# Performance work log

Measured on AMD Instinct MI355X. Metric: run time of the kernel, lower is better.

## Reference

```python
import jax, jax.numpy as jnp
import numpy as np

B, S, P, I = 32, 64, 32, 256
NF, H, L = 4, 512, 2
OUT = 2
INITRANGE = 0.1
assert NF * I == 2 * H  # layer-2 GRU input dim equals layer-1 input dim


def setup_inputs() -> dict:
    key = jax.random.key(0)
    ks = jax.random.split(key, 12)
    u = lambda k, shape: jax.random.uniform(k, shape, jnp.float32, -INITRANGE, INITRANGE)
    return {
        "inputs": jax.random.normal(ks[0], (B, S, P, I), jnp.float32),
        "inputs_demoip": jax.random.normal(ks[1], (B, 3), jnp.float32),
        "conv_w": u(ks[2], (NF, I)),            # Conv1d(1, NF, kernel=I) == dot product
        "conv_b": u(ks[3], (NF,)),
        "conv2_w": u(ks[4], (2 * H,)),          # Conv1d(1, 1, kernel=2H) == dot product
        "conv2_b": u(ks[5], (1,)),
        "wih": u(ks[6], (L, 2, 3 * H, NF * I)),  # [layer, dir, 3H, in]
        "whh": u(ks[7], (L, 2, 3 * H, H)),
        "bih": u(ks[8], (L, 2, 3 * H)),
        "bhh": u(ks[9], (L, 2, 3 * H)),
        "lin_w": u(ks[10], (OUT, 2 * H + 3)),
        "lin_b": u(ks[11], (OUT,)),
        "batch_size": B,
    }


def _gru_dir(x, wih, whh, bih, bhh, reverse):
    """One direction of a torch-style GRU. x: [B,S,in] -> [B,S,H]."""
    gx = jnp.einsum('bsi,gi->bsg', x, wih) + bih  # precompute input gates [B,S,3H]
    if reverse:
        gx = gx[:, ::-1]
    h0 = jnp.zeros((x.shape[0], H), x.dtype)

    def step(h, gxt):
        gh = h @ whh.T + bhh
        xr, xz, xn = jnp.split(gxt, 3, axis=-1)
        hr, hz, hn = jnp.split(gh, 3, axis=-1)
        r = jax.nn.sigmoid(xr + hr)
        z = jax.nn.sigmoid(xz + hz)
        n = jnp.tanh(xn + r * hn)
        h_new = (1.0 - z) * n + z * h
        return h_new, h_new

    _, ys = jax.lax.scan(step, h0, gx.transpose(1, 0, 2))
    ys = ys.transpose(1, 0, 2)  # [B,S,H]
    if reverse:
        ys = ys[:, ::-1]
    return ys


def reference(inputs, inputs_demoip, conv_w, conv_b, conv2_w, conv2_b,
              wih, whh, bih, bhh, lin_w, lin_b, batch_size):
    # --- convolutional attention embedding (kernel spans full input -> dot product) ---
    scores = jnp.einsum('bspi,fi->bsfp', inputs, conv_w) + conv_b[None, None, :, None]
    conv_wts = jax.nn.softmax(scores, axis=-1)                    # softmax over pad dim
    vec = jnp.einsum('bsfp,bspi->bsfi', conv_wts, inputs)         # [B,S,NF,I]
    embedding = vec.reshape(batch_size, S, NF * I)                # [B,S,NF*I]

    # --- stacked bidirectional GRU (eval mode: dropout omitted) ---
    x = embedding
    for l in range(L):
        f = _gru_dir(x, wih[l, 0], whh[l, 0], bih[l, 0], bhh[l, 0], False)
        b = _gru_dir(x, wih[l, 1], whh[l, 1], bih[l, 1], bhh[l, 1], True)
        x = jnp.concatenate([f, b], axis=-1)
    states = x                                                    # [B,S,2H]

    # --- second attention (conv2 kernel spans 2H -> dot product per step) ---
    alpha = jax.nn.softmax(states @ conv2_w + conv2_b[0], axis=1)  # [B,S]
    context = jnp.einsum('bs,bsh->bh', alpha, states)              # [B,2H]

    context_v2 = jnp.concatenate([context, inputs_demoip], axis=1)  # [B,2H+3]
    out = jax.nn.softmax(context_v2 @ lin_w.T + lin_b, axis=1)      # [B,OUT]
    return out, conv_wts, states, context, alpha
```

## Files before the change

kernel.cpp:

```cpp
#include <hip/hip_runtime.h>

typedef __attribute__((ext_vector_type(8))) short s8v;
typedef __attribute__((ext_vector_type(8))) __bf16 bf8v;
typedef __attribute__((ext_vector_type(4))) float f32x4;

#define DEVINL __device__ __forceinline__

DEVINL unsigned short f2bf(float f) {
    unsigned int x = __float_as_uint(f);
    unsigned int r = (x + 0x7FFFu + ((x >> 16) & 1u)) >> 16;
    return (unsigned short)r;
}

DEVINL f32x4 mfma16(s8v a, s8v b, f32x4 c) {
    return __builtin_amdgcn_mfma_f32_16x16x32_bf16(
        __builtin_bit_cast(bf8v, a), __builtin_bit_cast(bf8v, b), c, 0, 0, 0);
}

#define WS_CTR   0
#define WS_HBUF  4096
#define WS_ZERO_BYTES 266240
#define WS_WIH   266240
#define WS_WHH   (WS_WIH + 12582912)
#define WS_EMB   (WS_WHH + 6291456)
#define WS_ST1   (WS_EMB + 4194304)
#define WS_GX    (WS_ST1 + 4194304)

__global__ __launch_bounds__(256) void k_cvt(const float* __restrict__ in,
                                             unsigned short* __restrict__ out, int n) {
    int i0 = (blockIdx.x * 256 + threadIdx.x) * 8;
    if (i0 + 8 > n) return;
    f32x4 a = *(const f32x4*)(in + i0);
    f32x4 b = *(const f32x4*)(in + i0 + 4);
    s8v o;
    o[0] = (short)f2bf(a[0]); o[1] = (short)f2bf(a[1]);
    o[2] = (short)f2bf(a[2]); o[3] = (short)f2bf(a[3]);
    o[4] = (short)f2bf(b[0]); o[5] = (short)f2bf(b[1]);
    o[6] = (short)f2bf(b[2]); o[7] = (short)f2bf(b[3]);
    *(s8v*)(out + i0) = o;
}

__global__ __launch_bounds__(256) void k_conv(const float* __restrict__ inp,
                                              const float* __restrict__ conv_w,
                                              const float* __restrict__ conv_b,
                                              float* __restrict__ wts_out,
                                              unsigned short* __restrict__ emb) {
    const int bs = blockIdx.x, tid = threadIdx.x;
    __shared__ float xs[32][260];
    __shared__ float sc[4][32];
    __shared__ float wts[4][32];
    const float* x = inp + (size_t)bs * 8192;
    {
        int p = tid >> 3, i0 = (tid & 7) * 32;
        const float* src = x + p * 256 + i0;
        float* dst = &xs[p][i0];
#pragma unroll
        for (int j = 0; j < 32; j += 4) *(f32x4*)(dst + j) = *(const f32x4*)(src + j);
    }
    __syncthreads();
    {
        int p = tid >> 3, o = tid & 7;
        float s0 = 0, s1 = 0, s2 = 0, s3 = 0;
        const float* xp = &xs[p][o * 32];
#pragma unroll
        for (int j = 0; j < 32; j += 4) {
            f32x4 v  = *(const f32x4*)(xp + j);
            f32x4 w0 = *(const f32x4*)(conv_w + o * 32 + j);
            f32x4 w1 = *(const f32x4*)(conv_w + 256 + o * 32 + j);
            f32x4 w2 = *(const f32x4*)(conv_w + 512 + o * 32 + j);
            f32x4 w3 = *(const f32x4*)(conv_w + 768 + o * 32 + j);
#pragma unroll
            for (int q = 0; q < 4; ++q) {
                s0 += v[q] * w0[q]; s1 += v[q] * w1[q];
                s2 += v[q] * w2[q]; s3 += v[q] * w3[q];
            }
        }
#pragma unroll
        for (int d = 4; d; d >>= 1) {
            s0 += __shfl_down(s0, d, 8); s1 += __shfl_down(s1, d, 8);
            s2 += __shfl_down(s2, d, 8); s3 += __shfl_down(s3, d, 8);
        }
        if (o == 0) {
            sc[0][p] = s0 + conv_b[0]; sc[1][p] = s1 + conv_b[1];
            sc[2][p] = s2 + conv_b[2]; sc[3][p] = s3 + conv_b[3];
        }
    }
    __syncthreads();
    if (tid < 4) {
        float mx = -1e30f;
        for (int p = 0; p < 32; ++p) mx = fmaxf(mx, sc[tid][p]);
        float sm = 0.f;
        for (int p = 0; p < 32; ++p) { float e = __expf(sc[tid][p] - mx); wts[tid][p] = e; sm += e; }
        float inv = 1.f / sm;
        for (int p = 0; p < 32; ++p) wts[tid][p] *= inv;
    }
    __syncthreads();
    if (tid < 128) wts_out[(size_t)bs * 128 + tid] = wts[tid >> 5][tid & 31];
    {
        float a0 = 0, a1 = 0, a2 = 0, a3 = 0;
#pragma unroll 8
        for (int p = 0; p < 32; ++p) {
            float v = xs[p][tid];
            a0 += wts[0][p] * v; a1 += wts[1][p] * v;
            a2 += wts[2][p] * v; a3 += wts[3][p] * v;
        }
        unsigned short* e = emb + (size_t)bs * 1024;
        e[tid] = f2bf(a0); e[256 + tid] = f2bf(a1);
        e[512 + tid] = f2bf(a2); e[768 + tid] = f2bf(a3);
    }
}

__global__ __launch_bounds__(256, 2) void k_gemm(const unsigned short* __restrict__ A,
                                                 const unsigned short* __restrict__ B,
                                                 const float* __restrict__ bias,
                                                 const float* __restrict__ bias2,
                                                 float* __restrict__ C,
                                                 int M, int N, int K) {
    const int bm = blockIdx.y * 64, bn = blockIdx.x * 64;
    const int tid = threadIdx.x, w = tid >> 6, l = tid & 63;
    const int wm = (w >> 1) * 32, wn = (w & 1) * 32;
    __shared__ unsigned short As[64][72];
    __shared__ unsigned short Bs[64][72];
    f32x4 acc[2][2] = {};
    const int sr = tid >> 2;
    const int sk = (tid & 3) * 8;
    const int am = (l & 15), ak = (l >> 4) * 8;
    for (int k0 = 0; k0 < K; k0 += 64) {
        s8v a0 = *(const s8v*)(A + (size_t)(bm + sr) * K + k0 + sk);
        s8v a1 = *(const s8v*)(A + (size_t)(bm + sr) * K + k0 + sk + 32);
        s8v b0 = *(const s8v*)(B + (size_t)(bn + sr) * K + k0 + sk);
        s8v b1 = *(const s8v*)(B + (size_t)(bn + sr) * K + k0 + sk + 32);
        __syncthreads();
        *(s8v*)&As[sr][sk] = a0; *(s8v*)&As[sr][sk + 32] = a1;
        *(s8v*)&Bs[sr][sk] = b0; *(s8v*)&Bs[sr][sk + 32] = b1;
        __syncthreads();
#pragma unroll
        for (int kk = 0; kk < 64; kk += 32) {
            s8v fa0 = *(const s8v*)&As[wm + am][kk + ak];
            s8v fa1 = *(const s8v*)&As[wm + 16 + am][kk + ak];
            s8v fb0 = *(const s8v*)&Bs[wn + am][kk + ak];
            s8v fb1 = *(const s8v*)&Bs[wn + 16 + am][kk + ak];
            acc[0][0] = mfma16(fa0, fb0, acc[0][0]);
            acc[0][1] = mfma16(fa0, fb1, acc[0][1]);
            acc[1][0] = mfma16(fa1, fb0, acc[1][0]);
            acc[1][1] = mfma16(fa1, fb1, acc[1][1]);
        }
    }
#pragma unroll
    for (int mt = 0; mt < 2; ++mt)
#pragma unroll
        for (int nt = 0; nt < 2; ++nt)
#pragma unroll
            for (int r = 0; r < 4; ++r) {
                int row = bm + wm + mt * 16 + (l >> 4) * 4 + r;
                int col = bn + wn + nt * 16 + (l & 15);
                int gg = col >> 9;
                float b2 = (gg != 2 && gg != 5 && bias2) ? bias2[col] : 0.f;
                C[(size_t)row * N + col] = acc[mt][nt][r] + bias[col] + b2;
            }
}

__global__ __launch_bounds__(256, 1) void k_scan(const float* __restrict__ gx,
                                                 const unsigned short* __restrict__ whh,
                                                 const float* __restrict__ bhh,
                                                 unsigned short* __restrict__ hbuf,
                                                 unsigned int* __restrict__ flags,
                                                 float* __restrict__ st32,
                                                 unsigned short* __restrict__ st16) {
    const int sub = blockIdx.x & 7;
    if (sub > 1) return;
    const int dir = sub, jg = blockIdx.x >> 3;
    const int tid = threadIdx.x;
    const int w = tid >> 6, l = tid & 63;
    const int lr = l & 15, lq = l >> 4;
    const int jb = jg * 64;
    const int mycol = jb + w * 16 + lr;

    __shared__ __align__(1024) unsigned short hs[16384];

    s8v bf[3][16];
#pragma unroll
    for (int g = 0; g < 3; ++g) {
        const unsigned short* wr =
            whh + ((size_t)dir * 1536 + g * 512 + mycol) * 512 + lq * 8;
#pragma unroll
        for (int kt = 0; kt < 16; ++kt) bf[g][kt] = *(const s8v*)(wr + kt * 32);
    }
    const float bh_n = bhh[dir * 1536 + 1024 + mycol];

    unsigned short* hb0 = hbuf + (size_t)dir * 32768;
    unsigned int* fl = flags + dir * 128;
    unsigned int* myflag = fl + jg * 16;

    float hp[2][4] = {{0.f, 0.f, 0.f, 0.f}, {0.f, 0.f, 0.f, 0.f}};

    for (int t = 0; t < 64; ++t) {
        const int s = dir ? (63 - t) : t;
        float pg[3][2][4];
#pragma unroll
        for (int g = 0; g < 3; ++g)
#pragma unroll
            for (int bt = 0; bt < 2; ++bt)
#pragma unroll
                for (int r = 0; r < 4; ++r) {
                    const int b = bt * 16 + lq * 4 + r;
                    pg[g][bt][r] = gx[(size_t)(b * 64 + s) * 3072 + dir * 1536 +
                                      g * 512 + mycol];
                }
        if (t > 0) {
            if (w == 0 && l < 8) {
                while (__hip_atomic_load(&fl[l * 16], __ATOMIC_RELAXED,
                                         __HIP_MEMORY_SCOPE_AGENT) < (unsigned)t)
                    __builtin_amdgcn_s_sleep(1);
            }
            if (tid == 0)
                (void)__hip_atomic_load(&fl[0], __ATOMIC_ACQUIRE,
                                        __HIP_MEMORY_SCOPE_AGENT);
            __syncthreads();
        }
        const unsigned short* hc = hb0 + (size_t)(t & 1) * 16384;
#pragma unroll
        for (int i = 0; i < 8; ++i) {
            const int c = tid + 256 * i;
            const int row = c >> 6, inb = (c & 63) * 16;
            *(s8v*)((char*)hs + row * 1024 + (inb ^ ((row & 7) << 4))) =
                *(const s8v*)(hc + c * 8);
        }
        __syncthreads();
        f32x4 acc[3][2] = {};
#pragma unroll
        for (int bt = 0; bt < 2; ++bt) {
            const int row = bt * 16 + lr;
            const int m = (row & 7) << 4;
#pragma unroll
            for (int kt = 0; kt < 16; ++kt) {
                s8v a = *(const s8v*)((const char*)hs + row * 1024 +
                                      ((kt * 64 + lq * 16) ^ m));
                acc[0][bt] = mfma16(a, bf[0][kt], acc[0][bt]);
                acc[1][bt] = mfma16(a, bf[1][kt], acc[1][bt]);
                acc[2][bt] = mfma16(a, bf[2][kt], acc[2][bt]);
            }
        }
        unsigned short* hnw = hb0 + (size_t)((t + 1) & 1) * 16384;
        float hnew[2][4];
#pragma unroll
        for (int bt = 0; bt < 2; ++bt)
#pragma unroll
            for (int r = 0; r < 4; ++r) {
                const int b = bt * 16 + lq * 4 + r;
                float r_ = __builtin_amdgcn_rcpf(
                    1.f + __expf(-(pg[0][bt][r] + acc[0][bt][r])));
                float z_ = __builtin_amdgcn_rcpf(
                    1.f + __expf(-(pg[1][bt][r] + acc[1][bt][r])));
                float q = pg[2][bt][r] + r_ * (acc[2][bt][r] + bh_n);
                q = fminf(fmaxf(q, -15.f), 15.f);
                float e = __expf(2.f * q);
                float n_ = (e - 1.f) * __builtin_amdgcn_rcpf(e + 1.f);
                float h = (1.f - z_) * n_ + z_ * hp[bt][r];
                hp[bt][r] = h;
                hnew[bt][r] = h;
                __hip_atomic_store(&hnw[b * 512 + mycol], f2bf(h), __ATOMIC_RELAXED,
                                   __HIP_MEMORY_SCOPE_AGENT);
            }
        __syncthreads();
        if (tid == 0 && t < 63)
            __hip_atomic_store(myflag, (unsigned)(t + 1), __ATOMIC_RELEASE,
                               __HIP_MEMORY_SCOPE_AGENT);
#pragma unroll
        for (int bt = 0; bt < 2; ++bt)
#pragma unroll
            for (int r = 0; r < 4; ++r) {
                const int b = bt * 16 + lq * 4 + r;
                const size_t so = (size_t)(b * 64 + s) * 1024 + dir * 512 + mycol;
                if (st32) st32[so] = hnew[bt][r];
                if (st16) st16[so] = f2bf(hnew[bt][r]);
            }
    }
}

__global__ __launch_bounds__(256) void k_finale(const float* __restrict__ states,
                                                const float* __restrict__ conv2_w,
                                                const float* __restrict__ conv2_b,
                                                const float* __restrict__ demoip,
                                                const float* __restrict__ lin_w,
                                                const float* __restrict__ lin_b,
                                                float* __restrict__ out,
                                                float* __restrict__ context,
                                                float* __restrict__ alpha) {
    const int b = blockIdx.x, tid = threadIdx.x, w = tid >> 6, l = tid & 63;
    __shared__ float dots[64], al[64], ctx[1024], lg[2];
    const float* st = states + (size_t)b * 65536;
    for (int si = 0; si < 16; ++si) {
        int s = w * 16 + si;
        const float* row = st + s * 1024;
        float sum = 0.f;
        for (int i = l; i < 1024; i += 64) sum += row[i] * conv2_w[i];
#pragma unroll
        for (int m = 32; m; m >>= 1) sum += __shfl_xor(sum, m, 64);
        if (l == 0) dots[s] = sum + conv2_b[0];
    }
    __syncthreads();
    if (w == 0) {
        float v = dots[l];
        float mx = v;
#pragma unroll
        for (int m = 32; m; m >>= 1) mx = fmaxf(mx, __shfl_xor(mx, m, 64));
        float e = __expf(v - mx);
        float sm = e;
#pragma unroll
        for (int m = 32; m; m >>= 1) sm += __shfl_xor(sm, m, 64);
        float a = e / sm;
        al[l] = a;
        alpha[b * 64 + l] = a;
    }
    __syncthreads();
    for (int h = tid; h < 1024; h += 256) {
        float c = 0.f;
#pragma unroll 8
        for (int s = 0; s < 64; ++s) c += al[s] * st[s * 1024 + h];
        ctx[h] = c;
        context[b * 1024 + h] = c;
    }
    __syncthreads();
    if (w < 2) {
        const float* lw = lin_w + w * 1027;
        float sum = 0.f;
        for (int i = l; i < 1024; i += 64) sum += ctx[i] * lw[i];
#pragma unroll
        for (int m = 32; m; m >>= 1) sum += __shfl_xor(sum, m, 64);
        if (l == 0) {
            sum += lw[1024] * demoip[b * 3] + lw[1025] * demoip[b * 3 + 1] +
                   lw[1026] * demoip[b * 3 + 2] + lin_b[w];
            lg[w] = sum;
        }
    }
    __syncthreads();
    if (tid == 0) {
        float m = fmaxf(lg[0], lg[1]);
        float e0 = __expf(lg[0] - m), e1 = __expf(lg[1] - m);
        float inv = 1.f / (e0 + e1);
        out[b * 2 + 0] = e0 * inv;
        out[b * 2 + 1] = e1 * inv;
    }
}

extern "C" void kernel_launch(void* const* d_in, const int* in_sizes, int n_in,
                              void* d_out, int out_size, void* d_ws, size_t ws_size,
                              hipStream_t stream) {
    const float* inputs  = (const float*)d_in[0];
    const float* demoip  = (const float*)d_in[1];
    const float* conv_w  = (const float*)d_in[2];
    const float* conv_b  = (const float*)d_in[3];
    const float* conv2_w = (const float*)d_in[4];
    const float* conv2_b = (const float*)d_in[5];
    const float* wih     = (const float*)d_in[6];
    const float* whh     = (const float*)d_in[7];
    const float* bih     = (const float*)d_in[8];
    const float* bhh     = (const float*)d_in[9];
    const float* lin_w   = (const float*)d_in[10];
    const float* lin_b   = (const float*)d_in[11];

    char* ws = (char*)d_ws;
    unsigned int* ctrs    = (unsigned int*)(ws + WS_CTR);
    unsigned short* hbuf  = (unsigned short*)(ws + WS_HBUF);
    unsigned short* wih16 = (unsigned short*)(ws + WS_WIH);
    unsigned short* whh16 = (unsigned short*)(ws + WS_WHH);
    unsigned short* emb16 = (unsigned short*)(ws + WS_EMB);
    unsigned short* st116 = (unsigned short*)(ws + WS_ST1);
    float* gxbuf          = (float*)(ws + WS_GX);

    float* out_out    = (float*)d_out;
    float* wts_out    = out_out + 64;
    float* states_out = out_out + 262208;
    float* ctx_out    = out_out + 2359360;
    float* alpha_out  = out_out + 2392128;

    hipMemsetAsync(ws, 0, WS_ZERO_BYTES, stream);
    k_cvt<<<3072, 256, 0, stream>>>(wih, wih16, 6291456);
    k_cvt<<<1536, 256, 0, stream>>>(whh, whh16, 3145728);
    k_conv<<<2048, 256, 0, stream>>>(inputs, conv_w, conv_b, wts_out, emb16);
    k_gemm<<<dim3(48, 32), 256, 0, stream>>>(emb16, wih16, bih, bhh, gxbuf,
                                             2048, 3072, 1024);
    k_scan<<<64, 256, 0, stream>>>(gxbuf, whh16, bhh, hbuf, ctrs, nullptr, st116);
    k_gemm<<<dim3(48, 32), 256, 0, stream>>>(st116, wih16 + 3145728, bih + 3072,
                                             bhh + 3072, gxbuf, 2048, 3072, 1024);
    k_scan<<<64, 256, 0, stream>>>(gxbuf, whh16 + 1572864, bhh + 3072, hbuf + 65536,
                                   ctrs + 256, states_out, nullptr);
    k_finale<<<32, 256, 0, stream>>>(states_out, conv2_w, conv2_b, demoip, lin_w, lin_b,
                                     out_out, ctx_out, alpha_out);
}
```

Measured before the change: 944.7 us.

## Enlarge GEMM tiles with direct global-to-LDS loads and relax scan sync

The input-projection GEMM moves from 64x64 to 128x128 tiles, with 16 MFMA accumulators per wave. Tiles are staged through global_load_lds into an XOR-swizzled LDS layout, aiming for more reuse per LDS load and fewer register round-trips. The recurrent scan now launches only its 16 active blocks instead of 64 mostly-idle ones. Its acquire/release ordering is replaced by relaxed atomics with relaxed 64-bit atomic loads of the hidden state, which cuts synchronization overhead but could weaken memory-ordering guarantees between blocks.

```diff
diff --git a/kernel.cpp b/kernel.cpp
--- a/kernel.cpp
+++ b/kernel.cpp
@@ -3,6 +3,7 @@
 typedef __attribute__((ext_vector_type(8))) short s8v;
 typedef __attribute__((ext_vector_type(8))) __bf16 bf8v;
 typedef __attribute__((ext_vector_type(4))) float f32x4;
+typedef unsigned long long ULL;
 
 #define DEVINL __device__ __forceinline__
 
@@ -15,6 +16,12 @@
 DEVINL f32x4 mfma16(s8v a, s8v b, f32x4 c) {
     return __builtin_amdgcn_mfma_f32_16x16x32_bf16(
         __builtin_bit_cast(bf8v, a), __builtin_bit_cast(bf8v, b), c, 0, 0, 0);
+}
+
+typedef const __attribute__((address_space(1))) unsigned int gu32;
+typedef __attribute__((address_space(3))) unsigned int lu32;
+DEVINL void gload16(const void* g, unsigned int lds_off) {
+    __builtin_amdgcn_global_load_lds((gu32*)g, (lu32*)(size_t)lds_off, 16, 0, 0);
 }
 
 #define WS_CTR   0
@@ -116,46 +123,67 @@
                                                  const float* __restrict__ bias2,
                                                  float* __restrict__ C,
                                                  int M, int N, int K) {
-    const int bm = blockIdx.y * 64, bn = blockIdx.x * 64;
+    const int bm = blockIdx.y * 128, bn = blockIdx.x * 128;
     const int tid = threadIdx.x, w = tid >> 6, l = tid & 63;
-    const int wm = (w >> 1) * 32, wn = (w & 1) * 32;
-    __shared__ unsigned short As[64][72];
-    __shared__ unsigned short Bs[64][72];
-    f32x4 acc[2][2] = {};
-    const int sr = tid >> 2;
-    const int sk = (tid & 3) * 8;
-    const int am = (l & 15), ak = (l >> 4) * 8;
+    const int wr = w >> 1, wc = w & 1;
+    const int lr = l & 15, lq = l >> 4;
+
+    __shared__ __align__(1024) unsigned short As[8192];
+    __shared__ __align__(1024) unsigned short Bs[8192];
+    const unsigned int AsOff = (unsigned int)(size_t)(void*)As;
+    const unsigned int BsOff = (unsigned int)(size_t)(void*)Bs;
+
+    f32x4 acc[4][4] = {};
+    const int srow = tid >> 3;
+    const int scol = ((tid & 7) ^ (srow & 7)) * 8;
+    const unsigned int ldsW = w * 1024 + (l << 4);
+
     for (int k0 = 0; k0 < K; k0 += 64) {
-        s8v a0 = *(const s8v*)(A + (size_t)(bm + sr) * K + k0 + sk);
-        s8v a1 = *(const s8v*)(A + (size_t)(bm + sr) * K + k0 + sk + 32);
-        s8v b0 = *(const s8v*)(B + (size_t)(bn + sr) * K + k0 + sk);
-        s8v b1 = *(const s8v*)(B + (size_t)(bn + sr) * K + k0 + sk + 32);
         __syncthreads();
-        *(s8v*)&As[sr][sk] = a0; *(s8v*)&As[sr][sk + 32] = a1;
-        *(s8v*)&Bs[sr][sk] = b0; *(s8v*)&Bs[sr][sk + 32] = b1;
+#pragma unroll
+        for (int j = 0; j < 4; ++j)
+            gload16(A + (size_t)(bm + j * 32 + srow) * K + k0 + scol,
+                    AsOff + j * 4096 + (ldsW - (l << 4)));
+#pragma unroll
+        for (int j = 0; j < 4; ++j)
+            gload16(B + (size_t)(bn + j * 32 + srow) * K + k0 + scol,
+                    BsOff + j * 4096 + (ldsW - (l << 4)));
+        asm volatile("s_waitcnt vmcnt(0)" ::: "memory");
         __syncthreads();
 #pragma unroll
-        for (int kk = 0; kk < 64; kk += 32) {
-            s8v fa0 = *(const s8v*)&As[wm + am][kk + ak];
-            s8v fa1 = *(const s8v*)&As[wm + 16 + am][kk + ak];
-            s8v fb0 = *(const s8v*)&Bs[wn + am][kk + ak];
-            s8v fb1 = *(const s8v*)&Bs[wn + 16 + am][kk + ak];
-            acc[0][0] = mfma16(fa0, fb0, acc[0][0]);
-            acc[0][1] = mfma16(fa0, fb1, acc[0][1]);
-            acc[1][0] = mfma16(fa1, fb0, acc[1][0]);
-            acc[1][1] = mfma16(fa1, fb1, acc[1][1]);
-        }
-    }
-#pragma unroll
-    for (int mt = 0; mt < 2; ++mt)
-#pragma unroll
-        for (int nt = 0; nt < 2; ++nt)
+        for (int kk = 0; kk < 2; ++kk) {
+            s8v af[4], bf_[4];
+#pragma unroll
+            for (int mt = 0; mt < 4; ++mt) {
+                const int row = wr * 64 + mt * 16 + lr;
+                const int qg = kk * 4 + lq;
+                af[mt] = *(const s8v*)((const char*)As + row * 128 +
+                                       ((qg ^ (row & 7)) << 4));
+            }
+#pragma unroll
+            for (int nt = 0; nt < 4; ++nt) {
+                const int row = wc * 64 + nt * 16 + lr;
+                const int qg = kk * 4 + lq;
+                bf_[nt] = *(const s8v*)((const char*)Bs + row * 128 +
+                                        ((qg ^ (row & 7)) << 4));
+            }
+#pragma unroll
+            for (int mt = 0; mt < 4; ++mt)
+#pragma unroll
+                for (int nt = 0; nt < 4; ++nt)
+                    acc[mt][nt] = mfma16(af[mt], bf_[nt], acc[mt][nt]);
+        }
+    }
+#pragma unroll
+    for (int mt = 0; mt < 4; ++mt)
+#pragma unroll
+        for (int nt = 0; nt < 4; ++nt)
 #pragma unroll
             for (int r = 0; r < 4; ++r) {
-                int row = bm + wm + mt * 16 + (l >> 4) * 4 + r;
-                int col = bn + wn + nt * 16 + (l & 15);
+                int row = bm + wr * 64 + mt * 16 + lq * 4 + r;
+                int col = bn + wc * 64 + nt * 16 + lr;
                 int gg = col >> 9;
-                float b2 = (gg != 2 && gg != 5 && bias2) ? bias2[col] : 0.f;
+                float b2 = (gg != 2 && gg != 5) ? bias2[col] : 0.f;
                 C[(size_t)row * N + col] = acc[mt][nt][r] + bias[col] + b2;
             }
 }
@@ -167,9 +195,8 @@
                                                  unsigned int* __restrict__ flags,
                                                  float* __restrict__ st32,
                                                  unsigned short* __restrict__ st16) {
-    const int sub = blockIdx.x & 7;
-    if (sub > 1) return;
-    const int dir = sub, jg = blockIdx.x >> 3;
+    const int blk = blockIdx.x;
+    const int dir = blk >> 3, jg = blk & 7;
     const int tid = threadIdx.x;
     const int w = tid >> 6, l = tid & 63;
     const int lr = l & 15, lq = l >> 4;
@@ -213,9 +240,6 @@
                                          __HIP_MEMORY_SCOPE_AGENT) < (unsigned)t)
                     __builtin_amdgcn_s_sleep(1);
             }
-            if (tid == 0)
-                (void)__hip_atomic_load(&fl[0], __ATOMIC_ACQUIRE,
-                                        __HIP_MEMORY_SCOPE_AGENT);
             __syncthreads();
         }
         const unsigned short* hc = hb0 + (size_t)(t & 1) * 16384;
@@ -223,8 +247,12 @@
         for (int i = 0; i < 8; ++i) {
             const int c = tid + 256 * i;
             const int row = c >> 6, inb = (c & 63) * 16;
-            *(s8v*)((char*)hs + row * 1024 + (inb ^ ((row & 7) << 4))) =
-                *(const s8v*)(hc + c * 8);
+            const ULL* hq = (const ULL*)(hc + c * 8);
+            ULL d0 = __hip_atomic_load(hq, __ATOMIC_RELAXED, __HIP_MEMORY_SCOPE_AGENT);
+            ULL d1 = __hip_atomic_load(hq + 1, __ATOMIC_RELAXED, __HIP_MEMORY_SCOPE_AGENT);
+            char* dst = (char*)hs + row * 1024 + (inb ^ ((row & 7) << 4));
+            *(ULL*)dst = d0;
+            *(ULL*)(dst + 8) = d1;
         }
         __syncthreads();
         f32x4 acc[3][2] = {};
@@ -264,7 +292,7 @@
             }
         __syncthreads();
         if (tid == 0 && t < 63)
-            __hip_atomic_store(myflag, (unsigned)(t + 1), __ATOMIC_RELEASE,
+            __hip_atomic_store(myflag, (unsigned)(t + 1), __ATOMIC_RELAXED,
                                __HIP_MEMORY_SCOPE_AGENT);
 #pragma unroll
         for (int bt = 0; bt < 2; ++bt)
@@ -379,12 +407,12 @@
     k_cvt<<<3072, 256, 0, stream>>>(wih, wih16, 6291456);
     k_cvt<<<1536, 256, 0, stream>>>(whh, whh16, 3145728);
     k_conv<<<2048, 256, 0, stream>>>(inputs, conv_w, conv_b, wts_out, emb16);
-    k_gemm<<<dim3(48, 32), 256, 0, stream>>>(emb16, wih16, bih, bhh, gxbuf,
+    k_gemm<<<dim3(24, 16), 256, 0, stream>>>(emb16, wih16, bih, bhh, gxbuf,
                                              2048, 3072, 1024);
-    k_scan<<<64, 256, 0, stream>>>(gxbuf, whh16, bhh, hbuf, ctrs, nullptr, st116);
-    k_gemm<<<dim3(48, 32), 256, 0, stream>>>(st116, wih16 + 3145728, bih + 3072,
+    k_scan<<<16, 256, 0, stream>>>(gxbuf, whh16, bhh, hbuf, ctrs, nullptr, st116);
+    k_gemm<<<dim3(24, 16), 256, 0, stream>>>(st116, wih16 + 3145728, bih + 3072,
                                              bhh + 3072, gxbuf, 2048, 3072, 1024);
-    k_scan<<<64, 256, 0, stream>>>(gxbuf, whh16 + 1572864, bhh + 3072, hbuf + 65536,
+    k_scan<<<16, 256, 0, stream>>>(gxbuf, whh16 + 1572864, bhh + 3072, hbuf + 65536,
                                    ctrs + 256, states_out, nullptr);
     k_finale<<<32, 256, 0, stream>>>(states_out, conv2_w, conv2_b, demoip, lin_w, lin_b,
                                      out_out, ctx_out, alpha_out);
```

Measured after the change: 841.6 us. 10.9% less time.
